# Kernel tuning notes

Hardware: AMD Instinct MI355X
Metric: run time of the kernel (lower is better)

Reference implementation:

```python
import jax, jax.numpy as jnp
import numpy as np

B, S, H = 1, 2048, 3584
NH, NKV, D = 16, 8, 256
GROUPS = NH // NKV
WINDOW = 1024
SOFTCAP = 50.0
SCALING = 256.0 ** -0.5  # query_pre_attn_scalar ** -0.5
MASK_VAL = -1e9


def rotate_half(x):
    x1, x2 = jnp.split(x, 2, axis=-1)
    return jnp.concatenate([-x2, x1], axis=-1)


def setup_inputs() -> dict:
    key = jax.random.key(0)
    ks = jax.random.split(key, 5)
    hidden_states = jax.random.normal(ks[0], (B, S, H), dtype=jnp.float32)
    # real rotary embeddings, HF convention: [B, S, head_dim]
    inv_freq = 1.0 / (10000.0 ** (np.arange(0, D, 2, dtype=np.float32) / D))
    freqs = np.arange(S, dtype=np.float32)[:, None] * inv_freq[None, :]  # [S, D/2]
    emb = np.concatenate([freqs, freqs], axis=-1)  # [S, D]
    cos = jnp.asarray(np.cos(emb))[None]  # [1, S, D]
    sin = jnp.asarray(np.sin(emb))[None]
    sc = 1.0 / np.sqrt(H)
    wq = jax.random.normal(ks[1], (NH * D, H), dtype=jnp.float32) * sc
    wk = jax.random.normal(ks[2], (NKV * D, H), dtype=jnp.float32) * sc
    wv = jax.random.normal(ks[3], (NKV * D, H), dtype=jnp.float32) * sc
    wo = jax.random.normal(ks[4], (H, NH * D), dtype=jnp.float32) * (1.0 / np.sqrt(NH * D))
    return {"hidden_states": hidden_states, "cos": cos, "sin": sin,
            "wq": wq, "wk": wk, "wv": wv, "wo": wo}


def reference(hidden_states, cos, sin, wq, wk, wv, wo):
    # QKV projections -> [B, n_heads, S, D]
    q = jnp.einsum('bsh,oh->bso', hidden_states, wq).reshape(B, S, NH, D).transpose(0, 2, 1, 3)
    k = jnp.einsum('bsh,oh->bso', hidden_states, wk).reshape(B, S, NKV, D).transpose(0, 2, 1, 3)
    v = jnp.einsum('bsh,oh->bso', hidden_states, wv).reshape(B, S, NKV, D).transpose(0, 2, 1, 3)
    # RoPE (cos/sin broadcast over head dim)
    c = cos[:, None, :, :]
    s = sin[:, None, :, :]
    q = q * c + rotate_half(q) * s
    k = k * c + rotate_half(k) * s
    # GQA: repeat KV heads
    k = jnp.repeat(k, GROUPS, axis=1)  # [B, NH, S, D]
    v = jnp.repeat(v, GROUPS, axis=1)
    # scores + logit soft-capping (tanh), then causal + sliding-window mask
    scores = jnp.einsum('bhqd,bhkd->bhqk', q, k) * SCALING
    scores = SOFTCAP * jnp.tanh(scores / SOFTCAP)
    idx = jnp.arange(S)
    allowed = (idx[None, :] <= idx[:, None]) & (idx[:, None] - idx[None, :] < WINDOW)  # [S, S]
    scores = jnp.where(allowed[None, None], scores, MASK_VAL)
    p = jax.nn.softmax(scores, axis=-1)
    out = jnp.einsum('bhqk,bhkd->bhqd', p, v)  # [B, NH, S, D]
    out = out.transpose(0, 2, 1, 3).reshape(B, S, NH * D)
    return jnp.einsum('bso,ho->bsh', out, wo)
```

## Files before the change

### kernel.cpp

```cpp
#include <hip/hip_runtime.h>
#include <stdint.h>

#define S_LEN 2048
#define HDIM  3584
#define NHEAD 16
#define NKVH  8
#define DHEAD 256
#define QD    (NHEAD * DHEAD)
#define KD    (NKVH * DHEAD)
#define QKVD  (QD + 2 * KD)
#define WINDOW 1024
#define MASK_VAL (-1e9f)

typedef __bf16 bf16x8 __attribute__((ext_vector_type(8)));
typedef float  f32x4  __attribute__((ext_vector_type(4)));

__device__ __forceinline__ float bf2f(ushort u) {
    union { uint32_t i; float f; } v; v.i = ((uint32_t)u) << 16; return v.f;
}
__device__ __forceinline__ ushort f2bf(float f) {
    union { float f; uint32_t i; } v; v.f = f;
    uint32_t r = (v.i + 0x7FFF + ((v.i >> 16) & 1)) >> 16;
    return (ushort)r;
}
__device__ __forceinline__ void gll16(const ushort* g, ushort* l) {
    __builtin_amdgcn_global_load_lds(
        (const __attribute__((address_space(1))) void*)g,
        (__attribute__((address_space(3))) void*)l, 16, 0, 0);
}

#define N_H8  (S_LEN * HDIM / 8)
#define N_WQ8 (QD * HDIM / 8)
#define N_WK8 (KD * HDIM / 8)
#define N_WO8 (HDIM * QD / 8)
#define N_CVT (N_H8 + N_WQ8 + 2 * N_WK8 + N_WO8)

__global__ __launch_bounds__(256) void cvt5_kernel(
    const float* __restrict__ hid, const float* __restrict__ wq,
    const float* __restrict__ wk,  const float* __restrict__ wv,
    const float* __restrict__ wo,
    ushort* __restrict__ hb, ushort* __restrict__ wb, ushort* __restrict__ ob)
{
    int j = blockIdx.x * blockDim.x + threadIdx.x;
    const float* s; ushort* d;
    if (j < N_H8)                { s = hid; d = hb; }
    else if ((j -= N_H8) < N_WQ8)  { s = wq; d = wb; }
    else if ((j -= N_WQ8) < N_WK8) { s = wk; d = wb + (size_t)QD * HDIM; }
    else if ((j -= N_WK8) < N_WK8) { s = wv; d = wb + (size_t)(QD + KD) * HDIM; }
    else                         { j -= N_WK8; s = wo; d = ob; }
    float4 a = ((const float4*)s)[(size_t)j * 2];
    float4 b = ((const float4*)s)[(size_t)j * 2 + 1];
    ushort tmp[8];
    tmp[0] = f2bf(a.x); tmp[1] = f2bf(a.y); tmp[2] = f2bf(a.z); tmp[3] = f2bf(a.w);
    tmp[4] = f2bf(b.x); tmp[5] = f2bf(b.y); tmp[6] = f2bf(b.z); tmp[7] = f2bf(b.w);
    ((uint4*)d)[j] = *(uint4*)tmp;
}

__global__ __launch_bounds__(256) void cvt_kernel(const float* __restrict__ src,
                                                  ushort* __restrict__ dst, int n8)
{
    int i = blockIdx.x * blockDim.x + threadIdx.x;
    if (i >= n8) return;
    float4 a = ((const float4*)src)[i * 2];
    float4 b = ((const float4*)src)[i * 2 + 1];
    ushort tmp[8];
    tmp[0] = f2bf(a.x); tmp[1] = f2bf(a.y); tmp[2] = f2bf(a.z); tmp[3] = f2bf(a.w);
    tmp[4] = f2bf(b.x); tmp[5] = f2bf(b.y); tmp[6] = f2bf(b.z); tmp[7] = f2bf(b.w);
    ((uint4*)dst)[i] = *(uint4*)tmp;
}

__device__ __forceinline__ void stage_f32(ushort* __restrict__ dst,
                                          const float* __restrict__ src,
                                          int r0, int K, int kt, int t)
{
#pragma unroll
    for (int i = 0; i < 4; i++) {
        int g = t + i * 256;
        int row = g >> 3, c = g & 7;
        float4 f = *(const float4*)(src + (size_t)(r0 + row) * K + kt + c * 4);
        ushort4 u;
        u.x = f2bf(f.x); u.y = f2bf(f.y); u.z = f2bf(f.z); u.w = f2bf(f.w);
        int cl = (c >> 1) ^ ((row >> 1) & 3);
        *(ushort4*)(dst + row * 32 + cl * 8 + (c & 1) * 4) = u;
    }
}

#define VM4   asm volatile("s_waitcnt vmcnt(4)" ::: "memory")
#define VM3   asm volatile("s_waitcnt vmcnt(3)" ::: "memory")
#define VM0   asm volatile("s_waitcnt vmcnt(0)" ::: "memory")
#define MFEN  asm volatile("" ::: "memory")

#define MMAQ(AF, BF, QM, QN) do {                                              \
    __builtin_amdgcn_s_setprio(1);                                             \
    _Pragma("unroll") for (int i_ = 0; i_ < MIQ; i_++)                         \
      _Pragma("unroll") for (int n_ = 0; n_ < 2; n_++) {                       \
        acc[(QM) * MIQ + i_][(QN) * 2 + n_] = __builtin_amdgcn_mfma_f32_16x16x32_bf16( \
            AF[i_][0], BF[n_][0], acc[(QM) * MIQ + i_][(QN) * 2 + n_], 0, 0, 0);       \
        acc[(QM) * MIQ + i_][(QN) * 2 + n_] = __builtin_amdgcn_mfma_f32_16x16x32_bf16( \
            AF[i_][1], BF[n_][1], acc[(QM) * MIQ + i_][(QN) * 2 + n_], 0, 0, 0);       \
      }                                                                        \
    __builtin_amdgcn_s_setprio(0);                                             \
  } while (0)

template <int BM, typename TC>
__global__ __launch_bounds__(512, 2) void gemm256(const ushort* __restrict__ A,
                                                  const ushort* __restrict__ B,
                                                  TC* __restrict__ C,
                                                  int M, int N, int K)
{
    constexpr int WM  = BM / 2;
    constexpr int MIQ = WM / 32;
    __shared__ __align__(16) ushort As[2][BM * 64];
    __shared__ __align__(16) ushort Bs[2][256 * 64];

    const int t    = threadIdx.x;
    const int lane = t & 63;
    const int w    = t >> 6;
    const int l15  = lane & 15;
    const int quad = lane >> 4;
    const int m0   = blockIdx.y * BM;
    const int n0   = blockIdx.x * 256;
    const int wm   = (w >> 2) * WM;
    const int wn   = (w & 3) * 64;
    const int lr8  = lane >> 3;
    const int sc   = lane & 7;

    f32x4 acc[2 * MIQ][4] = {};
    bf16x8 a0f[MIQ][2], a1f[MIQ][2], b0f[2][2], b1f[2][2];

    auto readA = [&](bf16x8 (&af)[MIQ][2], int buf, int qm) {
#pragma unroll
        for (int i = 0; i < MIQ; i++) {
            int R = wm + qm * (WM / 2) + i * 16 + l15;
            af[i][0] = *(const bf16x8*)(&As[buf][R * 64 + ((quad ^ (R & 7)) * 8)]);
            af[i][1] = *(const bf16x8*)(&As[buf][R * 64 + (((4 + quad) ^ (R & 7)) * 8)]);
        }
    };
    auto readB = [&](bf16x8 (&bf)[2][2], int buf, int qn) {
#pragma unroll
        for (int n = 0; n < 2; n++) {
            int R = wn + qn * 32 + n * 16 + l15;
            bf[n][0] = *(const bf16x8*)(&Bs[buf][R * 64 + ((quad ^ (R & 7)) * 8)]);
            bf[n][1] = *(const bf16x8*)(&Bs[buf][R * 64 + (((4 + quad) ^ (R & 7)) * 8)]);
        }
    };

    auto stageA = [&](int buf, int qm, int tile) {
#pragma unroll
        for (int i = 0; i < BM / 128; i++) {
            int cb = (i * 8 + w) * 8;
            int lr = cb + lr8;
            int row, rb;
            if constexpr (BM == 256) {
                row = qm * 64 + (lr & 63) + ((lr >> 6) << 7);
                rb  = qm * 64 + (cb & 63) + ((cb >> 6) << 7);
            } else {
                row = qm * 32 + (lr & 31) + ((lr >> 5) << 6);
                rb  = qm * 32 + (cb & 31) + ((cb >> 5) << 6);
            }
            gll16(A + (size_t)(m0 + row) * K + tile * 64 + ((sc ^ lr8) * 8),
                  &As[buf][rb * 64]);
        }
    };
    auto stageB = [&](int buf, int qn, int tile) {
#pragma unroll
        for (int i = 0; i < 2; i++) {
            int cb  = (i * 8 + w) * 8;
            int lr  = cb + lr8;
            int row = ((lr >> 5) << 6) + qn * 32 + (lr & 31);
            int rb  = ((cb >> 5) << 6) + qn * 32 + (cb & 31);
            gll16(B + (size_t)(n0 + row) * K + tile * 64 + ((sc ^ lr8) * 8),
                  &Bs[buf][rb * 64]);
        }
    };

    const int NT = K >> 6;

    stageA(0, 0, 0); stageB(0, 0, 0); stageB(0, 1, 0); stageA(0, 1, 0);
    if constexpr (BM == 256) { VM4; } else { VM3; }
    __builtin_amdgcn_s_barrier(); MFEN;

    for (int T = 0; T < NT; ++T) {
        const int buf = T & 1;
        const bool pf = (T + 1 < NT);
        readB(b0f, buf, 0);
        readA(a0f, buf, 0);
        if (pf) { stageA(buf ^ 1, 0, T + 1); stageB(buf ^ 1, 0, T + 1); }
        MMAQ(a0f, b0f, 0, 0);
        if (pf) { if constexpr (BM == 256) { VM4; } else { VM3; } } else { VM0; }
        __builtin_amdgcn_s_barrier(); MFEN;
        readB(b1f, buf, 1);
        if (pf) { stageB(buf ^ 1, 1, T + 1); stageA(buf ^ 1, 1, T + 1); }
        MMAQ(a0f, b1f, 0, 1);
        readA(a1f, buf, 1);
        MMAQ(a1f, b1f, 1, 1);
        MMAQ(a1f, b0f, 1, 0);
        if (pf) {
            if constexpr (BM == 256) { VM4; } else { VM3; }
            __builtin_amdgcn_s_barrier(); MFEN;
        }
    }

#pragma unroll
    for (int qm = 0; qm < 2; qm++)
#pragma unroll
      for (int i = 0; i < MIQ; i++)
#pragma unroll
        for (int qn = 0; qn < 2; qn++)
#pragma unroll
          for (int n = 0; n < 2; n++)
#pragma unroll
            for (int r = 0; r < 4; r++) {
                int row = m0 + wm + qm * (WM / 2) + i * 16 + quad * 4 + r;
                int col = n0 + wn + qn * 32 + n * 16 + l15;
                float val = acc[qm * MIQ + i][qn * 2 + n][r];
                if constexpr (sizeof(TC) == 4) C[(size_t)row * N + col] = val;
                else                           C[(size_t)row * N + col] = f2bf(val);
            }
}

template <typename TA, typename TC>
__global__ __launch_bounds__(256) void gemm_async(const TA* __restrict__ A,
                                                  const ushort* __restrict__ B,
                                                  TC* __restrict__ C,
                                                  int M, int N, int K)
{
    __shared__ __align__(16) ushort As[128 * 32];
    __shared__ __align__(16) ushort Bs[128 * 32];

    const int t    = threadIdx.x;
    const int lane = t & 63;
    const int w    = t >> 6;
    const int l15  = lane & 15;
    const int quad = lane >> 4;
    const int m0   = blockIdx.y * 128;
    const int n0   = blockIdx.x * 128;
    const int wm   = (w >> 1) * 64;
    const int wn   = (w & 1) * 64;
    const int srow = lane >> 2;
    const int scol = ((lane & 3) ^ ((srow >> 1) & 3)) * 8;
    const int sw   = (l15 >> 1) & 3;

    f32x4 acc[4][4] = {};

    for (int kt = 0; kt < K; kt += 32) {
        __syncthreads();
#pragma unroll
        for (int j = 0; j < 2; j++) {
            const int rb = w * 32 + j * 16;
            if constexpr (sizeof(TA) == 2) {
                gll16((const ushort*)A + (size_t)(m0 + rb + srow) * K + kt + scol,
                      As + rb * 32);
            }
            gll16(B + (size_t)(n0 + rb + srow) * K + kt + scol, Bs + rb * 32);
        }
        if constexpr (sizeof(TA) == 4)
            stage_f32(As, (const float*)A, m0, K, kt, t);
        __syncthreads();

        bf16x8 a[4], b[4];
#pragma unroll
        for (int mi = 0; mi < 4; mi++)
            a[mi] = *(const bf16x8*)(As + (wm + mi * 16 + l15) * 32 + (quad ^ sw) * 8);
#pragma unroll
        for (int ni = 0; ni < 4; ni++)
            b[ni] = *(const bf16x8*)(Bs + (wn + ni * 16 + l15) * 32 + (quad ^ sw) * 8);
#pragma unroll
        for (int mi = 0; mi < 4; mi++)
#pragma unroll
            for (int ni = 0; ni < 4; ni++)
                acc[mi][ni] = __builtin_amdgcn_mfma_f32_16x16x32_bf16(
                    a[mi], b[ni], acc[mi][ni], 0, 0, 0);
    }

#pragma unroll
    for (int mi = 0; mi < 4; mi++)
#pragma unroll
        for (int ni = 0; ni < 4; ni++)
#pragma unroll
            for (int r = 0; r < 4; r++) {
                int row = m0 + wm + mi * 16 + quad * 4 + r;
                int col = n0 + wn + ni * 16 + l15;
                float val = acc[mi][ni][r];
                if constexpr (sizeof(TC) == 4) C[(size_t)row * N + col] = val;
                else                           C[(size_t)row * N + col] = f2bf(val);
            }
}

__global__ __launch_bounds__(256) void gemm_sync(const float* __restrict__ A,
                                                 const float* __restrict__ B,
                                                 ushort* __restrict__ C,
                                                 int M, int N, int K)
{
    __shared__ __align__(16) ushort As[128 * 32];
    __shared__ __align__(16) ushort Bs[128 * 32];
    const int t = threadIdx.x, lane = t & 63, w = t >> 6;
    const int l15 = lane & 15, quad = lane >> 4;
    const int sw = (l15 >> 1) & 3;
    const int m0 = blockIdx.y * 128, n0 = blockIdx.x * 128;
    const int wm = (w >> 1) * 64, wn = (w & 1) * 64;
    f32x4 acc[4][4] = {};
    for (int kt = 0; kt < K; kt += 32) {
        __syncthreads();
        stage_f32(As, A, m0, K, kt, t);
        stage_f32(Bs, B, n0, K, kt, t);
        __syncthreads();
        bf16x8 a[4], b[4];
#pragma unroll
        for (int mi = 0; mi < 4; mi++)
            a[mi] = *(const bf16x8*)(As + (wm + mi * 16 + l15) * 32 + (quad ^ sw) * 8);
#pragma unroll
        for (int ni = 0; ni < 4; ni++)
            b[ni] = *(const bf16x8*)(Bs + (wn + ni * 16 + l15) * 32 + (quad ^ sw) * 8);
#pragma unroll
        for (int mi = 0; mi < 4; mi++)
#pragma unroll
            for (int ni = 0; ni < 4; ni++)
                acc[mi][ni] = __builtin_amdgcn_mfma_f32_16x16x32_bf16(
                    a[mi], b[ni], acc[mi][ni], 0, 0, 0);
    }
#pragma unroll
    for (int mi = 0; mi < 4; mi++)
#pragma unroll
        for (int ni = 0; ni < 4; ni++)
#pragma unroll
            for (int r = 0; r < 4; r++)
                C[(size_t)(m0 + wm + mi * 16 + quad * 4 + r) * N +
                  n0 + wn + ni * 16 + l15] = f2bf(acc[mi][ni][r]);
}

__global__ __launch_bounds__(256) void gemm_sync_hf(const ushort* __restrict__ A,
                                                    const float* __restrict__ B,
                                                    float* __restrict__ C,
                                                    int M, int N, int K)
{
    __shared__ __align__(16) ushort As[128 * 32];
    __shared__ __align__(16) ushort Bs[128 * 32];
    const int t = threadIdx.x, lane = t & 63, w = t >> 6;
    const int l15 = lane & 15, quad = lane >> 4;
    const int sw = (l15 >> 1) & 3;
    const int m0 = blockIdx.y * 128, n0 = blockIdx.x * 128;
    const int wm = (w >> 1) * 64, wn = (w & 1) * 64;
    f32x4 acc[4][4] = {};
    for (int kt = 0; kt < K; kt += 32) {
        __syncthreads();
#pragma unroll
        for (int i = 0; i < 2; i++) {
            int g = t + i * 256;
            int row = g >> 2, c = g & 3;
            int cl = c ^ ((row >> 1) & 3);
            *(uint4*)(As + row * 32 + cl * 8) =
                *(const uint4*)(A + (size_t)(m0 + row) * K + kt + c * 8);
        }
        stage_f32(Bs, B, n0, K, kt, t);
        __syncthreads();
        bf16x8 a[4], b[4];
#pragma unroll
        for (int mi = 0; mi < 4; mi++)
            a[mi] = *(const bf16x8*)(As + (wm + mi * 16 + l15) * 32 + (quad ^ sw) * 8);
#pragma unroll
        for (int ni = 0; ni < 4; ni++)
            b[ni] = *(const bf16x8*)(Bs + (wn + ni * 16 + l15) * 32 + (quad ^ sw) * 8);
#pragma unroll
        for (int mi = 0; mi < 4; mi++)
#pragma unroll
            for (int ni = 0; ni < 4; ni++)
                acc[mi][ni] = __builtin_amdgcn_mfma_f32_16x16x32_bf16(
                    a[mi], b[ni], acc[mi][ni], 0, 0, 0);
    }
#pragma unroll
    for (int mi = 0; mi < 4; mi++)
#pragma unroll
        for (int ni = 0; ni < 4; ni++)
#pragma unroll
            for (int r = 0; r < 4; r++)
                C[(size_t)(m0 + wm + mi * 16 + quad * 4 + r) * N +
                  n0 + wn + ni * 16 + l15] = acc[mi][ni][r];
}

__global__ void rope_kernel(ushort* __restrict__ x, int stride,
                            const float* __restrict__ cosb,
                            const float* __restrict__ sinb, int nh)
{
    int idx  = blockIdx.x * blockDim.x + threadIdx.x;
    int d    = idx & 127;
    int rest = idx >> 7;
    int h    = rest & (nh - 1);
    int s    = rest / nh;
    size_t base = (size_t)s * stride + h * DHEAD;
    float c  = cosb[s * DHEAD + d];
    float sn = sinb[s * DHEAD + d];
    float x1 = bf2f(x[base + d]);
    float x2 = bf2f(x[base + d + 128]);
    x[base + d]       = f2bf(x1 * c - x2 * sn);
    x[base + d + 128] = f2bf(x2 * c + x1 * sn);
}

__global__ __launch_bounds__(256) void vtrans_kernel(const ushort* __restrict__ v,
                                                     int stride,
                                                     ushort* __restrict__ vt)
{
    __shared__ __align__(16) ushort tile[64][72];
    int s0 = blockIdx.x * 64, c0 = blockIdx.y * 64;
    int t  = threadIdx.x;
#pragma unroll
    for (int i = 0; i < 2; i++) {
        int cI = t + i * 256;
        int row = cI >> 3, c8 = cI & 7;
        *(uint4*)&tile[row][c8 * 8] =
            *(const uint4*)(v + (size_t)(s0 + row) * stride + c0 + c8 * 8);
    }
    __syncthreads();
#pragma unroll
    for (int i = 0; i < 2; i++) {
        int cI = t + i * 256;
        int crow = cI >> 3, s8 = cI & 7;
        ushort tmp[8];
#pragma unroll
        for (int j = 0; j < 8; j++) tmp[j] = tile[s8 * 8 + j][crow];
        *(uint4*)(vt + (size_t)(c0 + crow) * S_LEN + s0 + s8 * 8) = *(uint4*)tmp;
    }
}

template <typename TO>
__global__ __launch_bounds__(256) void attn_kernel(const ushort* __restrict__ qr, int qstride,
                                                   const ushort* __restrict__ kr, int kstride,
                                                   const ushort* __restrict__ vt,
                                                   TO* __restrict__ out)
{
    __shared__ __align__(16) ushort Ks[64 * 256];
    __shared__ __align__(16) ushort Vs[256 * 64];
    __shared__ __align__(16) ushort Ps[4][16 * 68];

    const int t    = threadIdx.x;
    const int lane = t & 63;
    const int w    = t >> 6;
    const int l15  = lane & 15;
    const int quad = lane >> 4;
    const int q0B  = blockIdx.x * 64;
    const int q0   = q0B + w * 16;
    const int h    = blockIdx.y;
    const int kvh  = h >> 1;

    bf16x8 aQ[8];
    const ushort* qrow = qr + (size_t)(q0 + l15) * qstride + h * DHEAD;
#pragma unroll
    for (int kk = 0; kk < 8; kk++)
        aQ[kk] = *(const bf16x8*)(qrow + kk * 32 + quad * 8);

    f32x4 oacc[16] = {};
    float m_i[4], l_i[4];
#pragma unroll
    for (int r = 0; r < 4; r++) { m_i[r] = -1e30f; l_i[r] = 0.f; }

    int km = q0B - (WINDOW - 1);
    if (km < 0) km = 0;
    km &= ~63;

    for (int kb = km; kb < q0B + 64; kb += 64) {
        __syncthreads();
#pragma unroll
        for (int i = 0; i < 8; i++) {
            int base = i * 256 + w * 64;
            int idx  = base + lane;
            int row = idx >> 5, c = idx & 31;
            int cs = c ^ (row & 7);
            gll16(kr + (size_t)(kb + row) * kstride + kvh * DHEAD + cs * 8,
                  Ks + base * 8);
        }
#pragma unroll
        for (int i = 0; i < 8; i++) {
            int base = i * 256 + w * 64;
            int idx  = base + lane;
            int row = idx >> 3, c = idx & 7;
            int cs = c ^ (row & 7);
            gll16(vt + (size_t)(kvh * DHEAD + row) * S_LEN + kb + cs * 8,
                  Vs + base * 8);
        }
        __syncthreads();

        f32x4 sc[4] = {};
#pragma unroll
        for (int ni = 0; ni < 4; ni++) {
            int row = ni * 16 + l15;
#pragma unroll
            for (int kk = 0; kk < 8; kk++) {
                int cp = (kk * 4 + quad) ^ (row & 7);
                bf16x8 bk = *(const bf16x8*)(Ks + row * 256 + cp * 8);
                sc[ni] = __builtin_amdgcn_mfma_f32_16x16x32_bf16(aQ[kk], bk, sc[ni], 0, 0, 0);
            }
        }

        const bool interior = (kb + 63 <= q0) && (q0 + 15 - kb < WINDOW);
        float p[4][4];
        float mt[4] = { -1e30f, -1e30f, -1e30f, -1e30f };
        if (interior) {
#pragma unroll
            for (int ni = 0; ni < 4; ni++)
#pragma unroll
                for (int r = 0; r < 4; r++) {
                    float e = __expf(sc[ni][r] * 0.0025f);
                    float x = 50.f * (e - 1.f) * __builtin_amdgcn_rcpf(e + 1.f);
                    p[ni][r] = x;
                    mt[r] = fmaxf(mt[r], x);
                }
        } else {
#pragma unroll
            for (int ni = 0; ni < 4; ni++)
#pragma unroll
                for (int r = 0; r < 4; r++) {
                    int qi = q0 + quad * 4 + r;
                    int ki = kb + ni * 16 + l15;
                    float e = __expf(sc[ni][r] * 0.0025f);
                    float x = 50.f * (e - 1.f) * __builtin_amdgcn_rcpf(e + 1.f);
                    bool ok = (ki <= qi) && (qi - ki < WINDOW);
                    x = ok ? x : MASK_VAL;
                    p[ni][r] = x;
                    mt[r] = fmaxf(mt[r], x);
                }
        }
#pragma unroll
        for (int r = 0; r < 4; r++)
#pragma unroll
            for (int off = 1; off < 16; off <<= 1)
                mt[r] = fmaxf(mt[r], __shfl_xor(mt[r], off));

        float alpha[4], rs[4];
#pragma unroll
        for (int r = 0; r < 4; r++) {
            float mn = fmaxf(m_i[r], mt[r]);
            alpha[r] = __expf(m_i[r] - mn);
            m_i[r] = mn;
            rs[r] = 0.f;
        }
#pragma unroll
        for (int ni = 0; ni < 4; ni++)
#pragma unroll
            for (int r = 0; r < 4; r++) {
                float pe = __expf(p[ni][r] - m_i[r]);
                rs[r] += pe;
                Ps[w][(quad * 4 + r) * 68 + ni * 16 + l15] = f2bf(pe);
            }
#pragma unroll
        for (int r = 0; r < 4; r++) {
#pragma unroll
            for (int off = 1; off < 16; off <<= 1)
                rs[r] += __shfl_xor(rs[r], off);
            l_i[r] = l_i[r] * alpha[r] + rs[r];
        }
#pragma unroll
        for (int nd = 0; nd < 16; nd++)
#pragma unroll
            for (int r = 0; r < 4; r++)
                oacc[nd][r] *= alpha[r];

        __asm__ volatile("s_waitcnt lgkmcnt(0)" ::: "memory");

        bf16x8 aP[2];
#pragma unroll
        for (int kk = 0; kk < 2; kk++)
            aP[kk] = *(const bf16x8*)(&Ps[w][l15 * 68 + kk * 32 + quad * 8]);
#pragma unroll
        for (int nd = 0; nd < 16; nd++) {
            int row = nd * 16 + l15;
#pragma unroll
            for (int kk = 0; kk < 2; kk++) {
                int cp = (kk * 4 + quad) ^ (row & 7);
                bf16x8 bv = *(const bf16x8*)(Vs + row * 64 + cp * 8);
                oacc[nd] = __builtin_amdgcn_mfma_f32_16x16x32_bf16(aP[kk], bv, oacc[nd], 0, 0, 0);
            }
        }
    }

#pragma unroll
    for (int r = 0; r < 4; r++) {
        float invl = __builtin_amdgcn_rcpf(l_i[r]);
#pragma unroll
        for (int nd = 0; nd < 16; nd++) {
            int qi = q0 + quad * 4 + r;
            int d  = nd * 16 + l15;
            float val = oacc[nd][r] * invl;
            if constexpr (sizeof(TO) == 4) out[(size_t)qi * QD + h * DHEAD + d] = val;
            else                           out[(size_t)qi * QD + h * DHEAD + d] = f2bf(val);
        }
    }
}

extern "C" void kernel_launch(void* const* d_in, const int* in_sizes, int n_in,
                              void* d_out, int out_size, void* d_ws, size_t ws_size,
                              hipStream_t stream)
{
    const float* hidden = (const float*)d_in[0];
    const float* cosb   = (const float*)d_in[1];
    const float* sinb   = (const float*)d_in[2];
    const float* wq     = (const float*)d_in[3];
    const float* wk     = (const float*)d_in[4];
    const float* wv     = (const float*)d_in[5];
    const float* wo     = (const float*)d_in[6];
    float* outp = (float*)d_out;

    const size_t nH   = (size_t)S_LEN * HDIM;
    const size_t nWQ  = (size_t)QD * HDIM;
    const size_t nWK  = (size_t)KD * HDIM;
    const size_t nWB  = (size_t)QKVD * HDIM;
    const size_t nWO  = (size_t)HDIM * QD;
    const size_t nQKV = (size_t)S_LEN * QKVD;
    const size_t nAT  = (size_t)S_LEN * QD;
    const size_t nVT  = (size_t)S_LEN * KD;

    dim3 blk(256);
    dim3 blk512(512);
    const size_t needA = (nWB + nQKV + nH + nWO) * 2;
    const size_t needB = (nWB + nQKV) * 2;

    if (ws_size >= needA) {
        ushort* wb  = (ushort*)d_ws;
        ushort* qkv = wb + nWB;
        ushort* hb  = qkv + nQKV;
        ushort* ob  = hb + nH;
        ushort* at  = wb;
        ushort* vtb = wb + nAT;

        cvt5_kernel<<<(N_CVT + 255) / 256, blk, 0, stream>>>(hidden, wq, wk, wv, wo, hb, wb, ob);
        gemm256<256, ushort><<<dim3(QKVD / 256, S_LEN / 256), blk512, 0, stream>>>(
            hb, wb, qkv, S_LEN, QKVD, HDIM);
        rope_kernel<<<(S_LEN * NHEAD * 128) / 256, blk, 0, stream>>>(qkv, QKVD, cosb, sinb, NHEAD);
        rope_kernel<<<(S_LEN * NKVH * 128) / 256, blk, 0, stream>>>(qkv + QD, QKVD, cosb, sinb, NKVH);
        vtrans_kernel<<<dim3(S_LEN / 64, KD / 64), blk, 0, stream>>>(qkv + QD + KD, QKVD, vtb);
        attn_kernel<ushort><<<dim3(S_LEN / 64, NHEAD), blk, 0, stream>>>(
            qkv, QKVD, qkv + QD, QKVD, vtb, at);
        gemm256<128, float><<<dim3(HDIM / 256, S_LEN / 128), blk512, 0, stream>>>(
            at, ob, outp, S_LEN, HDIM, QD);
    } else if (ws_size >= needB) {
        ushort* wb  = (ushort*)d_ws;
        ushort* qkv = wb + nWB;
        ushort* at  = wb;
        ushort* vtb = wb + nAT;
        ushort* ob  = wb + nAT + nVT;

        cvt_kernel<<<(int)(nWQ / 8 / 256), blk, 0, stream>>>(wq, wb, (int)(nWQ / 8));
        cvt_kernel<<<(int)(nWK / 8 / 256), blk, 0, stream>>>(wk, wb + nWQ, (int)(nWK / 8));
        cvt_kernel<<<(int)(nWK / 8 / 256), blk, 0, stream>>>(wv, wb + nWQ + nWK, (int)(nWK / 8));
        gemm_async<float, ushort><<<dim3(QKVD / 128, S_LEN / 128), blk, 0, stream>>>(
            hidden, wb, qkv, S_LEN, QKVD, HDIM);
        cvt_kernel<<<(int)(nWO / 8 / 256), blk, 0, stream>>>(wo, ob, (int)(nWO / 8));
        rope_kernel<<<(S_LEN * NHEAD * 128) / 256, blk, 0, stream>>>(qkv, QKVD, cosb, sinb, NHEAD);
        rope_kernel<<<(S_LEN * NKVH * 128) / 256, blk, 0, stream>>>(qkv + QD, QKVD, cosb, sinb, NKVH);
        vtrans_kernel<<<dim3(S_LEN / 64, KD / 64), blk, 0, stream>>>(qkv + QD + KD, QKVD, vtb);
        attn_kernel<ushort><<<dim3(S_LEN / 64, NHEAD), blk, 0, stream>>>(
            qkv, QKVD, qkv + QD, QKVD, vtb, at);
        gemm256<128, float><<<dim3(HDIM / 256, S_LEN / 128), blk512, 0, stream>>>(
            at, ob, outp, S_LEN, HDIM, QD);
    } else {
        ushort* q   = (ushort*)d_ws;
        ushort* k   = q + nAT;
        ushort* v   = k + nVT;
        ushort* vtb = v + nVT;
        ushort* at  = vtb + nVT;

        gemm_sync<<<dim3(QD / 128, S_LEN / 128), blk, 0, stream>>>(hidden, wq, q, S_LEN, QD, HDIM);
        gemm_sync<<<dim3(KD / 128, S_LEN / 128), blk, 0, stream>>>(hidden, wk, k, S_LEN, KD, HDIM);
        gemm_sync<<<dim3(KD / 128, S_LEN / 128), blk, 0, stream>>>(hidden, wv, v, S_LEN, KD, HDIM);
        rope_kernel<<<(S_LEN * NHEAD * 128) / 256, blk, 0, stream>>>(q, QD, cosb, sinb, NHEAD);
        rope_kernel<<<(S_LEN * NKVH * 128) / 256, blk, 0, stream>>>(k, KD, cosb, sinb, NKVH);
        vtrans_kernel<<<dim3(S_LEN / 64, KD / 64), blk, 0, stream>>>(v, KD, vtb);
        attn_kernel<ushort><<<dim3(S_LEN / 64, NHEAD), blk, 0, stream>>>(q, QD, k, KD, vtb, at);
        gemm_sync_hf<<<dim3(HDIM / 128, S_LEN / 128), blk, 0, stream>>>(at, wo, outp, S_LEN, HDIM, QD);
    }
}
```

Baseline: 547.0 us.

## Add 8-phase pipelined 256x256 GEMM kernel for QKV projection

Adds a new 256x256-tile bf16 MFMA GEMM for the QKV projection. Each K-tile of 64 is split into quarter-tile phases, with global-to-LDS loads for upcoming quarters issued between MFMA phases and barriers after each phase. It reuses A/B fragment registers across phases so fewer LDS reads are needed. The aim is finer overlap of memory loads with MFMA work. The cost is more barriers and complex waitcnt bookkeeping that could stall or be subtly wrong. The old kernel is renamed and kept for the output projection.

```diff
diff --git a/kernel.cpp b/kernel.cpp
--- a/kernel.cpp
+++ b/kernel.cpp
@@ -85,10 +85,134 @@
     }
 }
 
+#define VM6   asm volatile("s_waitcnt vmcnt(6)" ::: "memory")
 #define VM4   asm volatile("s_waitcnt vmcnt(4)" ::: "memory")
 #define VM3   asm volatile("s_waitcnt vmcnt(3)" ::: "memory")
 #define VM0   asm volatile("s_waitcnt vmcnt(0)" ::: "memory")
+#define LGKM0 asm volatile("s_waitcnt lgkmcnt(0)" ::: "memory")
 #define MFEN  asm volatile("" ::: "memory")
+
+#define PHASE_A(BUF, AF, BF, LA, LB, QM, QN, STAGE, TWAIT) do {                \
+    if (LA) {                                                                  \
+      _Pragma("unroll") for (int i_ = 0; i_ < 4; i_++) {                       \
+        int R_ = wm + (QM) * 64 + i_ * 16 + l15;                               \
+        AF[i_][0] = *(const bf16x8*)(&As[BUF][R_ * 64 + ((quad ^ (R_ & 7)) * 8)]);       \
+        AF[i_][1] = *(const bf16x8*)(&As[BUF][R_ * 64 + (((4 + quad) ^ (R_ & 7)) * 8)]); \
+      }                                                                        \
+    }                                                                          \
+    if (LB) {                                                                  \
+      _Pragma("unroll") for (int n_ = 0; n_ < 2; n_++) {                       \
+        int R_ = wn + (QN) * 32 + n_ * 16 + l15;                               \
+        BF[n_][0] = *(const bf16x8*)(&Bs[BUF][R_ * 64 + ((quad ^ (R_ & 7)) * 8)]);       \
+        BF[n_][1] = *(const bf16x8*)(&Bs[BUF][R_ * 64 + (((4 + quad) ^ (R_ & 7)) * 8)]); \
+      }                                                                        \
+    }                                                                          \
+    STAGE;                                                                     \
+    MFEN;                                                                      \
+    __builtin_amdgcn_s_barrier();                                              \
+    LGKM0;                                                                     \
+    __builtin_amdgcn_s_setprio(1);                                             \
+    _Pragma("unroll") for (int i_ = 0; i_ < 4; i_++)                           \
+      _Pragma("unroll") for (int n_ = 0; n_ < 2; n_++) {                       \
+        acc[(QM) * 4 + i_][(QN) * 2 + n_] = __builtin_amdgcn_mfma_f32_16x16x32_bf16(  \
+            AF[i_][0], BF[n_][0], acc[(QM) * 4 + i_][(QN) * 2 + n_], 0, 0, 0);        \
+        acc[(QM) * 4 + i_][(QN) * 2 + n_] = __builtin_amdgcn_mfma_f32_16x16x32_bf16(  \
+            AF[i_][1], BF[n_][1], acc[(QM) * 4 + i_][(QN) * 2 + n_], 0, 0, 0);        \
+      }                                                                        \
+    __builtin_amdgcn_s_setprio(0);                                             \
+    TWAIT;                                                                     \
+    __builtin_amdgcn_s_barrier();                                              \
+    MFEN;                                                                      \
+  } while (0)
+
+template <typename TC>
+__global__ __launch_bounds__(512, 2) void gemm256x256(const ushort* __restrict__ A,
+                                                      const ushort* __restrict__ B,
+                                                      TC* __restrict__ C,
+                                                      int M, int N, int K)
+{
+    __shared__ __align__(16) ushort As[2][256 * 64];
+    __shared__ __align__(16) ushort Bs[2][256 * 64];
+
+    const int t    = threadIdx.x;
+    const int lane = t & 63;
+    const int w    = t >> 6;
+    const int l15  = lane & 15;
+    const int quad = lane >> 4;
+    const int m0   = blockIdx.y * 256;
+    const int n0   = blockIdx.x * 256;
+    const int wm   = (w >> 2) * 128;
+    const int wn   = (w & 3) * 64;
+    const int lr8  = lane >> 3;
+    const int sc   = lane & 7;
+
+    f32x4 acc[8][4] = {};
+    bf16x8 a0f[4][2], a1f[4][2], b0f[2][2], b1f[2][2];
+
+    auto stageA = [&](int buf, int qm, int tile) {
+#pragma unroll
+        for (int i = 0; i < 2; i++) {
+            int cb  = (i * 8 + w) * 8;
+            int lr  = cb + lr8;
+            int row = qm * 64 + (lr & 63) + ((lr >> 6) << 7);
+            int rb  = qm * 64 + (cb & 63) + ((cb >> 6) << 7);
+            gll16(A + (size_t)(m0 + row) * K + tile * 64 + ((sc ^ lr8) * 8),
+                  &As[buf][rb * 64]);
+        }
+    };
+    auto stageB = [&](int buf, int qn, int tile) {
+#pragma unroll
+        for (int i = 0; i < 2; i++) {
+            int cb  = (i * 8 + w) * 8;
+            int lr  = cb + lr8;
+            int row = ((lr >> 5) << 6) + qn * 32 + (lr & 31);
+            int rb  = ((cb >> 5) << 6) + qn * 32 + (cb & 31);
+            gll16(B + (size_t)(n0 + row) * K + tile * 64 + ((sc ^ lr8) * 8),
+                  &Bs[buf][rb * 64]);
+        }
+    };
+
+    stageB(0, 0, 0);
+    stageA(0, 1, 0);
+    stageA(0, 0, 0);
+    stageB(0, 1, 0);
+    stageB(1, 0, 1);
+    stageA(1, 1, 1);
+    VM6;
+    __builtin_amdgcn_s_barrier();
+    MFEN;
+
+    const int NJ = K >> 7;
+    for (int j = 0; j < NJ; ++j) {
+        const int T = 2 * j;
+        const bool tl = (j == NJ - 1);
+        PHASE_A(0, a0f, b0f, 1, 1, 0, 0, stageA(1, 0, T + 1), MFEN);
+        PHASE_A(0, a1f, b0f, 1, 0, 1, 0, stageB(1, 1, T + 1), if (tl) { VM0; } else { VM6; });
+        PHASE_A(0, a1f, b1f, 0, 1, 1, 1, if (!tl) { stageB(0, 0, T + 2); }, MFEN);
+        PHASE_A(0, a0f, b1f, 0, 0, 0, 1, if (!tl) { stageA(0, 1, T + 2); }, if (!tl) { VM6; } else { MFEN; });
+        PHASE_A(1, a0f, b0f, 1, 1, 0, 0, if (!tl) { stageA(0, 0, T + 2); }, MFEN);
+        PHASE_A(1, a1f, b0f, 1, 0, 1, 0, if (!tl) { stageB(0, 1, T + 2); }, if (!tl) { VM6; } else { MFEN; });
+        PHASE_A(1, a1f, b1f, 0, 1, 1, 1, if (!tl) { stageB(1, 0, T + 3); }, MFEN);
+        PHASE_A(1, a0f, b1f, 0, 0, 0, 1, if (!tl) { stageA(1, 1, T + 3); }, if (!tl) { VM6; } else { MFEN; });
+    }
+
+#pragma unroll
+    for (int qm = 0; qm < 2; qm++)
+#pragma unroll
+      for (int i = 0; i < 4; i++)
+#pragma unroll
+        for (int qn = 0; qn < 2; qn++)
+#pragma unroll
+          for (int n = 0; n < 2; n++)
+#pragma unroll
+            for (int r = 0; r < 4; r++) {
+                int row = m0 + wm + qm * 64 + i * 16 + quad * 4 + r;
+                int col = n0 + wn + qn * 32 + n * 16 + l15;
+                float val = acc[qm * 4 + i][qn * 2 + n][r];
+                if constexpr (sizeof(TC) == 4) C[(size_t)row * N + col] = val;
+                else                           C[(size_t)row * N + col] = f2bf(val);
+            }
+}
 
 #define MMAQ(AF, BF, QM, QN) do {                                              \
     __builtin_amdgcn_s_setprio(1);                                             \
@@ -103,10 +227,10 @@
   } while (0)
 
 template <int BM, typename TC>
-__global__ __launch_bounds__(512, 2) void gemm256(const ushort* __restrict__ A,
-                                                  const ushort* __restrict__ B,
-                                                  TC* __restrict__ C,
-                                                  int M, int N, int K)
+__global__ __launch_bounds__(512, 2) void gemm2b(const ushort* __restrict__ A,
+                                                 const ushort* __restrict__ B,
+                                                 TC* __restrict__ C,
+                                                 int M, int N, int K)
 {
     constexpr int WM  = BM / 2;
     constexpr int MIQ = WM / 32;
@@ -622,14 +746,14 @@
         ushort* vtb = wb + nAT;
 
         cvt5_kernel<<<(N_CVT + 255) / 256, blk, 0, stream>>>(hidden, wq, wk, wv, wo, hb, wb, ob);
-        gemm256<256, ushort><<<dim3(QKVD / 256, S_LEN / 256), blk512, 0, stream>>>(
+        gemm256x256<ushort><<<dim3(QKVD / 256, S_LEN / 256), blk512, 0, stream>>>(
             hb, wb, qkv, S_LEN, QKVD, HDIM);
         rope_kernel<<<(S_LEN * NHEAD * 128) / 256, blk, 0, stream>>>(qkv, QKVD, cosb, sinb, NHEAD);
         rope_kernel<<<(S_LEN * NKVH * 128) / 256, blk, 0, stream>>>(qkv + QD, QKVD, cosb, sinb, NKVH);
         vtrans_kernel<<<dim3(S_LEN / 64, KD / 64), blk, 0, stream>>>(qkv + QD + KD, QKVD, vtb);
         attn_kernel<ushort><<<dim3(S_LEN / 64, NHEAD), blk, 0, stream>>>(
             qkv, QKVD, qkv + QD, QKVD, vtb, at);
-        gemm256<128, float><<<dim3(HDIM / 256, S_LEN / 128), blk512, 0, stream>>>(
+        gemm2b<128, float><<<dim3(HDIM / 256, S_LEN / 128), blk512, 0, stream>>>(
             at, ob, outp, S_LEN, HDIM, QD);
     } else if (ws_size >= needB) {
         ushort* wb  = (ushort*)d_ws;
@@ -649,7 +773,7 @@
         vtrans_kernel<<<dim3(S_LEN / 64, KD / 64), blk, 0, stream>>>(qkv + QD + KD, QKVD, vtb);
         attn_kernel<ushort><<<dim3(S_LEN / 64, NHEAD), blk, 0, stream>>>(
             qkv, QKVD, qkv + QD, QKVD, vtb, at);
-        gemm256<128, float><<<dim3(HDIM / 256, S_LEN / 128), blk512, 0, stream>>>(
+        gemm2b<128, float><<<dim3(HDIM / 256, S_LEN / 128), blk512, 0, stream>>>(
             at, ob, outp, S_LEN, HDIM, QD);
     } else {
         ushort* q   = (ushort*)d_ws;
```

New measurement: 525.2 us. 1.04x faster.
